# Kernel optimization log

Hardware: AMD Instinct MI355X
Metric: run time of the kernel (lower is better)

## Reference

```python
import jax, jax.numpy as jnp
import numpy as np

D = 1024
H = 16
HD = D // H
FF = 4 * D
EPS = 1e-6


def layernorm(x, g, b):
    mu = jnp.mean(x, axis=-1, keepdims=True)
    var = jnp.mean((x - mu) ** 2, axis=-1, keepdims=True)
    return (x - mu) * jax.lax.rsqrt(var + EPS) * g + b


def setup_inputs() -> dict:
    key = jax.random.key(0)
    ks = jax.random.split(key, 12)
    s = 0.02
    return {
        "x": jax.random.normal(ks[0], (8, 1024, D), dtype=jnp.float32),
        "qkv_w": jax.random.normal(ks[1], (3 * D, D), dtype=jnp.float32) * s,
        "qkv_b": jnp.zeros((3 * D,), dtype=jnp.float32),
        "proj_w": jax.random.normal(ks[2], (D, D), dtype=jnp.float32) * s,
        "proj_b": jnp.zeros((D,), dtype=jnp.float32),
        "fc1_w": jax.random.normal(ks[3], (FF, D), dtype=jnp.float32) * s,
        "fc1_b": jnp.zeros((FF,), dtype=jnp.float32),
        "fc2_w": jax.random.normal(ks[4], (D, FF), dtype=jnp.float32) * s,
        "fc2_b": jnp.zeros((D,), dtype=jnp.float32),
        "ln1_g": jnp.ones((D,), dtype=jnp.float32),
        "ln1_b": jnp.zeros((D,), dtype=jnp.float32),
        "ln2_g": jnp.ones((D,), dtype=jnp.float32),
        "ln2_b": jnp.zeros((D,), dtype=jnp.float32),
    }


def reference(x, qkv_w, qkv_b, proj_w, proj_b, fc1_w, fc1_b, fc2_w, fc2_b,
              ln1_g, ln1_b, ln2_g, ln2_b):
    B, S, _ = x.shape
    # attention branch
    h = layernorm(x, ln1_g, ln1_b)
    qkv = h @ qkv_w.T + qkv_b                      # [B,S,3D]
    qkv = qkv.reshape(B, S, 3, H, HD)
    q, k, v = qkv[:, :, 0], qkv[:, :, 1], qkv[:, :, 2]  # [B,S,H,HD]
    scores = jnp.einsum('bshd,bthd->bhst', q, k) * (HD ** -0.5)
    attn = jax.nn.softmax(scores, axis=-1)
    ctx = jnp.einsum('bhst,bthd->bshd', attn, v).reshape(B, S, D)
    x = x + ctx @ proj_w.T + proj_b
    # mlp branch
    h = layernorm(x, ln2_g, ln2_b)
    h = jax.nn.gelu(h @ fc1_w.T + fc1_b, approximate=False)
    x = x + h @ fc2_w.T + fc2_b
    return x
```

## Files before the change

kernel.cpp:

```cpp
#include <hip/hip_runtime.h>
#include <stdint.h>

typedef unsigned short u16;
typedef __attribute__((ext_vector_type(8))) short bf16x8;
typedef __attribute__((ext_vector_type(4))) short bf16x4;
typedef __attribute__((ext_vector_type(4))) float f32x4;

__device__ __forceinline__ u16 f2bf(float f) {
    union { float f; uint32_t u; } v; v.f = f;
    uint32_t r = (v.u + 0x7FFFu + ((v.u >> 16) & 1u)) >> 16;
    return (u16)r;
}

__device__ __forceinline__ void g2l16(const u16* g, u16* l) {
    __builtin_amdgcn_global_load_lds(
        (const __attribute__((address_space(1))) uint32_t*)g,
        (__attribute__((address_space(3))) uint32_t*)l, 16, 0, 0);
}

__device__ __forceinline__ float gelu_f(float x) {
    float x2 = x * x;
    float u = x * (0.7978845608028654f + 0.035677408136300125f * x2);
    float t = exp2f(-2.8853900817779268f * fabsf(u));
    float th = (1.0f - t) / (1.0f + t);
    th = (u < 0.0f) ? -th : th;
    return 0.5f * x * (1.0f + th);
}

__global__ __launch_bounds__(256) void cvt_kernel(const float* __restrict__ in,
                                                  u16* __restrict__ out, int n4) {
    int i = blockIdx.x * 256 + threadIdx.x;
    if (i < n4) {
        float4 v = ((const float4*)in)[i];
        uint2 o;
        o.x = (uint32_t)f2bf(v.x) | ((uint32_t)f2bf(v.y) << 16);
        o.y = (uint32_t)f2bf(v.z) | ((uint32_t)f2bf(v.w) << 16);
        ((uint2*)out)[i] = o;
    }
}

__global__ __launch_bounds__(256) void ln_kernel(const float* __restrict__ x,
                                                 const float* __restrict__ g,
                                                 const float* __restrict__ beta,
                                                 u16* __restrict__ out) {
    int row = blockIdx.x;
    int tid = threadIdx.x;
    const float4 v = ((const float4*)(x + (size_t)row * 1024))[tid];
    float s  = v.x + v.y + v.z + v.w;
    float sq = v.x*v.x + v.y*v.y + v.z*v.z + v.w*v.w;
    #pragma unroll
    for (int off = 32; off; off >>= 1) {
        s  += __shfl_xor(s,  off, 64);
        sq += __shfl_xor(sq, off, 64);
    }
    __shared__ float rs[4], rq[4];
    int w = tid >> 6;
    if ((tid & 63) == 0) { rs[w] = s; rq[w] = sq; }
    __syncthreads();
    s  = rs[0] + rs[1] + rs[2] + rs[3];
    sq = rq[0] + rq[1] + rq[2] + rq[3];
    float mu   = s * (1.0f / 1024.0f);
    float var  = sq * (1.0f / 1024.0f) - mu * mu;
    float rstd = rsqrtf(var + 1e-6f);
    float4 gv = ((const float4*)g)[tid];
    float4 bv = ((const float4*)beta)[tid];
    uint2 o;
    o.x = (uint32_t)f2bf((v.x - mu) * rstd * gv.x + bv.x) |
          ((uint32_t)f2bf((v.y - mu) * rstd * gv.y + bv.y) << 16);
    o.y = (uint32_t)f2bf((v.z - mu) * rstd * gv.z + bv.z) |
          ((uint32_t)f2bf((v.w - mu) * rstd * gv.w + bv.w) << 16);
    ((uint2*)(out + (size_t)row * 1024))[tid] = o;
}

template<int M_REP, int ACT, int RES, int OUTBF>
__global__ __launch_bounds__(512, 2) void gemm2_kernel(
    const u16* __restrict__ A, const u16* __restrict__ W,
    const float* __restrict__ bias, const float* __restrict__ res,
    void* __restrict__ Cout, int M, int N, int K)
{
    const int BM = M_REP * 32;
    __shared__ u16 sA[2 * BM * 64];
    __shared__ u16 sB[2 * 256 * 64];

    int tid = threadIdx.x;
    int lane = tid & 63, wid = tid >> 6;
    int wm = wid >> 2, wn = wid & 3;
    int q = lane & 15, g = lane >> 4;

    int MT = M / BM;
    int nwg = gridDim.x;
    int chunk = nwg >> 3;
    int bid = blockIdx.x;
    int wg = (bid & 7) * chunk + (bid >> 3);
    int mt = wg % MT, nt = wg / MT;
    int m0 = mt * BM, n0 = nt * 256;

    const int NT = K >> 6;

    f32x4 acc[M_REP][4] = {};

    auto STAGE = [&](int buf, int k0) {
        #pragma unroll
        for (int l = 0; l < BM / 64; l++) {
            int idx = l * 512 + tid;
            int row = idx >> 3;
            int col = ((idx & 7) * 8) ^ ((row & 7) << 3);
            g2l16(A + (size_t)(m0 + row) * K + k0 + col,
                  sA + buf * (BM * 64) + (l * 512 + wid * 64) * 8);
        }
        #pragma unroll
        for (int l = 0; l < 4; l++) {
            int idx = l * 512 + tid;
            int row = idx >> 3;
            int col = ((idx & 7) * 8) ^ ((row & 7) << 3);
            g2l16(W + (size_t)(n0 + row) * K + k0 + col,
                  sB + buf * (256 * 64) + (l * 512 + wid * 64) * 8);
        }
    };

    STAGE(0, 0);
    __syncthreads();

    int buf = 0;
    for (int t = 0; t < NT; t++) {
        if (t + 1 < NT) STAGE(buf ^ 1, (t + 1) << 6);
        const u16* bA = sA + buf * (BM * 64);
        const u16* bB = sB + buf * (256 * 64);
        #pragma unroll
        for (int ks = 0; ks < 2; ks++) {
            bf16x8 af[M_REP], bfr[4];
            #pragma unroll
            for (int i = 0; i < M_REP; i++) {
                int rowL = wm * (BM / 2) + i * 16 + q;
                int colE = (ks * 32 + g * 8) ^ ((rowL & 7) << 3);
                af[i] = *(const bf16x8*)(bA + rowL * 64 + colE);
            }
            #pragma unroll
            for (int j = 0; j < 4; j++) {
                int rowL = wn * 64 + j * 16 + q;
                int colE = (ks * 32 + g * 8) ^ ((rowL & 7) << 3);
                bfr[j] = *(const bf16x8*)(bB + rowL * 64 + colE);
            }
            #pragma unroll
            for (int i = 0; i < M_REP; i++)
                #pragma unroll
                for (int j = 0; j < 4; j++)
                    acc[i][j] = __builtin_amdgcn_mfma_f32_16x16x32_bf16(af[i], bfr[j], acc[i][j], 0, 0, 0);
        }
        __syncthreads();
        buf ^= 1;
    }

    #pragma unroll
    for (int i = 0; i < M_REP; i++) {
        #pragma unroll
        for (int j = 0; j < 4; j++) {
            int col = n0 + wn * 64 + j * 16 + q;
            float bz = bias[col];
            #pragma unroll
            for (int r = 0; r < 4; r++) {
                int row = m0 + wm * (BM / 2) + i * 16 + g * 4 + r;
                float v = acc[i][j][r] + bz;
                if (ACT == 1) v = gelu_f(v);
                if (RES) v += res[(size_t)row * N + col];
                if (OUTBF) ((u16*)Cout)[(size_t)row * N + col] = f2bf(v);
                else       ((float*)Cout)[(size_t)row * N + col] = v;
            }
        }
    }
}

__global__ __launch_bounds__(256) void attn_kernel(const u16* __restrict__ qkv,
                                                   u16* __restrict__ ctx) {
    int bid = blockIdx.x;
    int qt = bid & 15;
    int h  = (bid >> 4) & 15;
    int b  = bid >> 8;
    int tid = threadIdx.x, lane = tid & 63, w = tid >> 6;
    int q = lane & 15, g = lane >> 4;

    __shared__ u16 sQ[64 * 72];
    __shared__ u16 sK[32 * 72];
    __shared__ u16 sVT[64 * 36];

    const size_t tokBase = ((size_t)b * 1024) * 3072 + (size_t)h * 64;
    const float SC = 0.125f * 1.44269504088896f;

    #pragma unroll
    for (int p = 0; p < 2; p++) {
        int flat = (p * 256 + tid) * 8;
        int r = flat >> 6, c = flat & 63;
        uint4 v = *(const uint4*)(qkv + tokBase + (size_t)(qt * 64 + r) * 3072 + c);
        *(uint4*)(sQ + r * 72 + c) = v;
    }
    __syncthreads();
    bf16x8 qf0 = *(const bf16x8*)(sQ + (w * 16 + q) * 72 + g * 8);
    bf16x8 qf1 = *(const bf16x8*)(sQ + (w * 16 + q) * 72 + 32 + g * 8);

    float m_run = -1e30f, l_run = 0.0f;
    f32x4 o[4];
    #pragma unroll
    for (int n = 0; n < 4; n++) o[n] = (f32x4){0.f, 0.f, 0.f, 0.f};

    int kr = tid >> 3, kc = (tid & 7) * 8;
    int kperm = ((kr >> 2) & 3) * 8 + (kr >> 4) * 4 + (kr & 3);

    for (int kt = 0; kt < 32; kt++) {
        __syncthreads();
        {
            uint4 v = *(const uint4*)(qkv + tokBase + (size_t)(kt * 32 + kperm) * 3072 + 1024 + kc);
            *(uint4*)(sK + kr * 72 + kc) = v;
        }
        #pragma unroll
        for (int p = 0; p < 2; p++) {
            int flat = (p * 256 + tid) * 4;
            int key = flat >> 6, cc = flat & 63;
            ushort4 vv = *(const ushort4*)(qkv + tokBase + (size_t)(kt * 32 + key) * 3072 + 2048 + cc);
            sVT[(cc + 0) * 36 + key] = vv.x;
            sVT[(cc + 1) * 36 + key] = vv.y;
            sVT[(cc + 2) * 36 + key] = vv.z;
            sVT[(cc + 3) * 36 + key] = vv.w;
        }
        __syncthreads();

        f32x4 s0 = (f32x4){0.f, 0.f, 0.f, 0.f}, s1 = s0;
        {
            bf16x8 k00 = *(const bf16x8*)(sK + (q) * 72 + g * 8);
            bf16x8 k01 = *(const bf16x8*)(sK + (q) * 72 + 32 + g * 8);
            s0 = __builtin_amdgcn_mfma_f32_16x16x32_bf16(k00, qf0, s0, 0, 0, 0);
            s0 = __builtin_amdgcn_mfma_f32_16x16x32_bf16(k01, qf1, s0, 0, 0, 0);
            bf16x8 k10 = *(const bf16x8*)(sK + (16 + q) * 72 + g * 8);
            bf16x8 k11 = *(const bf16x8*)(sK + (16 + q) * 72 + 32 + g * 8);
            s1 = __builtin_amdgcn_mfma_f32_16x16x32_bf16(k10, qf0, s1, 0, 0, 0);
            s1 = __builtin_amdgcn_mfma_f32_16x16x32_bf16(k11, qf1, s1, 0, 0, 0);
        }
        float ps[8];
        #pragma unroll
        for (int r = 0; r < 4; r++) { ps[r] = s0[r] * SC; ps[4 + r] = s1[r] * SC; }
        float tm = ps[0];
        #pragma unroll
        for (int i = 1; i < 8; i++) tm = fmaxf(tm, ps[i]);
        tm = fmaxf(tm, __shfl_xor(tm, 16, 64));
        tm = fmaxf(tm, __shfl_xor(tm, 32, 64));

        if (!__all(tm - m_run <= 8.0f)) {
            float nm = fmaxf(m_run, tm);
            float f = exp2f(m_run - nm);
            float fr[4];
            #pragma unroll
            for (int r = 0; r < 4; r++) fr[r] = __shfl(f, g * 4 + r, 64);
            #pragma unroll
            for (int n = 0; n < 4; n++)
                #pragma unroll
                for (int r = 0; r < 4; r++) o[n][r] *= fr[r];
            l_run *= f;
            m_run = nm;
        }

        float ts = 0.0f;
        #pragma unroll
        for (int i = 0; i < 8; i++) { ps[i] = exp2f(ps[i] - m_run); ts += ps[i]; }
        ts += __shfl_xor(ts, 16, 64);
        ts += __shfl_xor(ts, 32, 64);
        l_run += ts;

        bf16x8 pf;
        #pragma unroll
        for (int j = 0; j < 8; j++) pf[j] = (short)f2bf(ps[j]);

        #pragma unroll
        for (int n = 0; n < 4; n++) {
            bf16x4 vlo = *(const bf16x4*)(sVT + (n * 16 + q) * 36 + g * 8);
            bf16x4 vhi = *(const bf16x4*)(sVT + (n * 16 + q) * 36 + g * 8 + 4);
            bf16x8 vf;
            #pragma unroll
            for (int j = 0; j < 4; j++) { vf[j] = vlo[j]; vf[4 + j] = vhi[j]; }
            o[n] = __builtin_amdgcn_mfma_f32_16x16x32_bf16(pf, vf, o[n], 0, 0, 0);
        }
    }

    float inv = 1.0f / l_run;
    float ir[4];
    #pragma unroll
    for (int r = 0; r < 4; r++) ir[r] = __shfl(inv, g * 4 + r, 64);
    size_t outBase = ((size_t)b * 1024 + qt * 64 + w * 16) * 1024 + (size_t)h * 64;
    #pragma unroll
    for (int n = 0; n < 4; n++)
        #pragma unroll
        for (int r = 0; r < 4; r++)
            ctx[outBase + (size_t)(g * 4 + r) * 1024 + n * 16 + q] = f2bf(o[n][r] * ir[r]);
}

extern "C" void kernel_launch(void* const* d_in, const int* in_sizes, int n_in,
                              void* d_out, int out_size, void* d_ws, size_t ws_size,
                              hipStream_t stream) {
    const float* x      = (const float*)d_in[0];
    const float* qkv_w  = (const float*)d_in[1];
    const float* qkv_b  = (const float*)d_in[2];
    const float* proj_w = (const float*)d_in[3];
    const float* proj_b = (const float*)d_in[4];
    const float* fc1_w  = (const float*)d_in[5];
    const float* fc1_b  = (const float*)d_in[6];
    const float* fc2_w  = (const float*)d_in[7];
    const float* fc2_b  = (const float*)d_in[8];
    const float* ln1_g  = (const float*)d_in[9];
    const float* ln1_b  = (const float*)d_in[10];
    const float* ln2_g  = (const float*)d_in[11];
    const float* ln2_b  = (const float*)d_in[12];
    float* out = (float*)d_out;

    char* ws = (char*)d_ws;
    u16* wq = (u16*)(ws);
    u16* wp = (u16*)(ws + 6291456);
    u16* w1 = (u16*)(ws + 8388608);
    u16* w2 = (u16*)(ws + 16777216);
    char* pool = ws + 25165824;
    u16* hbuf = (u16*)(pool);
    u16* qkvb = (u16*)(pool + 16777216);
    u16* ctxb = (u16*)(pool);
    u16* h2b  = (u16*)(pool + 16777216);
    u16* a1b  = (u16*)(pool + 33554432);

    cvt_kernel<<<3072, 256, 0, stream>>>(qkv_w, wq, 786432);
    cvt_kernel<<<1024, 256, 0, stream>>>(proj_w, wp, 262144);
    cvt_kernel<<<4096, 256, 0, stream>>>(fc1_w, w1, 1048576);
    cvt_kernel<<<4096, 256, 0, stream>>>(fc2_w, w2, 1048576);

    ln_kernel<<<8192, 256, 0, stream>>>(x, ln1_g, ln1_b, hbuf);
    gemm2_kernel<4,0,0,1><<<768, 512, 0, stream>>>(hbuf, wq, qkv_b, nullptr, qkvb, 8192, 3072, 1024);
    attn_kernel<<<2048, 256, 0, stream>>>(qkvb, ctxb);
    gemm2_kernel<4,0,1,0><<<256, 512, 0, stream>>>(ctxb, wp, proj_b, x, out, 8192, 1024, 1024);
    ln_kernel<<<8192, 256, 0, stream>>>(out, ln2_g, ln2_b, h2b);
    gemm2_kernel<8,1,0,1><<<512, 512, 0, stream>>>(h2b, w1, fc1_b, nullptr, a1b, 8192, 4096, 1024);
    gemm2_kernel<4,0,1,0><<<256, 512, 0, stream>>>(a1b, w2, fc2_b, out, out, 8192, 1024, 4096);
}
```

Before: 563.2 us.

## Triple-stage GEMM prefetch, write V transposed from QKV GEMM, double-buffer attention tiles

The GEMM now issues the loads for stage t+2 right after the fragments are read, using explicit waitcnt and barriers in place of a single-stage prefetch. The tile is fixed at 128x256, so the fc1 GEMM drops from 256-row tiles to 128-row tiles with twice the workgroups, and the occupancy hint of two workgroups per CU is removed. The QKV GEMM epilogue writes V transposed into a separate buffer, so attention no longer does a scalar LDS transpose. Attention processes 64-key tiles with register-staged double buffering of K and V. The risks are hand-managed vmcnt counts, more register pressure, and scattered 8-byte stores when writing the transposed V.

```diff
diff --git a/kernel.cpp b/kernel.cpp
--- a/kernel.cpp
+++ b/kernel.cpp
@@ -3,7 +3,6 @@
 
 typedef unsigned short u16;
 typedef __attribute__((ext_vector_type(8))) short bf16x8;
-typedef __attribute__((ext_vector_type(4))) short bf16x4;
 typedef __attribute__((ext_vector_type(4))) float f32x4;
 
 __device__ __forceinline__ u16 f2bf(float f) {
@@ -72,105 +71,135 @@
     ((uint2*)(out + (size_t)row * 1024))[tid] = o;
 }
 
-template<int M_REP, int ACT, int RES, int OUTBF>
-__global__ __launch_bounds__(512, 2) void gemm2_kernel(
+template<int ACT, int RES, int OUTMODE>
+__global__ __launch_bounds__(512) void gemm2_kernel(
     const u16* __restrict__ A, const u16* __restrict__ W,
     const float* __restrict__ bias, const float* __restrict__ res,
-    void* __restrict__ Cout, int M, int N, int K)
+    void* __restrict__ Cout, u16* __restrict__ vtb, int M, int N, int K)
 {
-    const int BM = M_REP * 32;
-    __shared__ u16 sA[2 * BM * 64];
-    __shared__ u16 sB[2 * 256 * 64];
+    const int BM = 128, BN = 256, BK = 64;
+    __shared__ u16 sA[2 * BM * BK];
+    __shared__ u16 sB[2 * BN * BK];
 
     int tid = threadIdx.x;
     int lane = tid & 63, wid = tid >> 6;
     int wm = wid >> 2, wn = wid & 3;
     int q = lane & 15, g = lane >> 4;
 
-    int MT = M / BM;
+    int MT = M >> 7;
     int nwg = gridDim.x;
     int chunk = nwg >> 3;
     int bid = blockIdx.x;
     int wg = (bid & 7) * chunk + (bid >> 3);
     int mt = wg % MT, nt = wg / MT;
-    int m0 = mt * BM, n0 = nt * 256;
-
+    int m0 = mt << 7, n0 = nt << 8;
     const int NT = K >> 6;
 
-    f32x4 acc[M_REP][4] = {};
-
-    auto STAGE = [&](int buf, int k0) {
-        #pragma unroll
-        for (int l = 0; l < BM / 64; l++) {
-            int idx = l * 512 + tid;
-            int row = idx >> 3;
-            int col = ((idx & 7) * 8) ^ ((row & 7) << 3);
-            g2l16(A + (size_t)(m0 + row) * K + k0 + col,
-                  sA + buf * (BM * 64) + (l * 512 + wid * 64) * 8);
-        }
-        #pragma unroll
-        for (int l = 0; l < 4; l++) {
-            int idx = l * 512 + tid;
-            int row = idx >> 3;
-            int col = ((idx & 7) * 8) ^ ((row & 7) << 3);
-            g2l16(W + (size_t)(n0 + row) * K + k0 + col,
-                  sB + buf * (256 * 64) + (l * 512 + wid * 64) * 8);
-        }
-    };
+    const u16* srcA[2]; const u16* srcB[4];
+    u16* dstA[2]; u16* dstB[4];
+    #pragma unroll
+    for (int l = 0; l < 2; l++) {
+        int idx = l * 512 + tid, row = idx >> 3;
+        int col = ((idx & 7) * 8) ^ ((row & 7) << 3);
+        srcA[l] = A + (size_t)(m0 + row) * K + col;
+        dstA[l] = sA + (l * 512 + wid * 64) * 8;
+    }
+    #pragma unroll
+    for (int l = 0; l < 4; l++) {
+        int idx = l * 512 + tid, row = idx >> 3;
+        int col = ((idx & 7) * 8) ^ ((row & 7) << 3);
+        srcB[l] = W + (size_t)(n0 + row) * K + col;
+        dstB[l] = sB + (l * 512 + wid * 64) * 8;
+    }
+
+    #define STAGE(bf, t) { int ko = (t) * 64; int boA = (bf) * (BM * BK); int boB = (bf) * (BN * BK); \
+        g2l16(srcA[0] + ko, dstA[0] + boA); g2l16(srcA[1] + ko, dstA[1] + boA); \
+        g2l16(srcB[0] + ko, dstB[0] + boB); g2l16(srcB[1] + ko, dstB[1] + boB); \
+        g2l16(srcB[2] + ko, dstB[2] + boB); g2l16(srcB[3] + ko, dstB[3] + boB); }
+
+    f32x4 acc[4][4] = {};
 
     STAGE(0, 0);
-    __syncthreads();
+    STAGE(1, 1);
+    asm volatile("s_waitcnt vmcnt(6)\n" ::: "memory");
+    __builtin_amdgcn_s_barrier();
 
     int buf = 0;
     for (int t = 0; t < NT; t++) {
-        if (t + 1 < NT) STAGE(buf ^ 1, (t + 1) << 6);
-        const u16* bA = sA + buf * (BM * 64);
-        const u16* bB = sB + buf * (256 * 64);
+        const u16* bA = sA + buf * (BM * BK);
+        const u16* bB = sB + buf * (BN * BK);
+        bf16x8 af[2][4], bfr[2][4];
         #pragma unroll
         for (int ks = 0; ks < 2; ks++) {
-            bf16x8 af[M_REP], bfr[4];
-            #pragma unroll
-            for (int i = 0; i < M_REP; i++) {
-                int rowL = wm * (BM / 2) + i * 16 + q;
+            #pragma unroll
+            for (int i = 0; i < 4; i++) {
+                int rowL = wm * 64 + i * 16 + q;
                 int colE = (ks * 32 + g * 8) ^ ((rowL & 7) << 3);
-                af[i] = *(const bf16x8*)(bA + rowL * 64 + colE);
+                af[ks][i] = *(const bf16x8*)(bA + rowL * 64 + colE);
             }
             #pragma unroll
             for (int j = 0; j < 4; j++) {
                 int rowL = wn * 64 + j * 16 + q;
                 int colE = (ks * 32 + g * 8) ^ ((rowL & 7) << 3);
-                bfr[j] = *(const bf16x8*)(bB + rowL * 64 + colE);
+                bfr[ks][j] = *(const bf16x8*)(bB + rowL * 64 + colE);
             }
-            #pragma unroll
-            for (int i = 0; i < M_REP; i++)
+        }
+        asm volatile("s_waitcnt lgkmcnt(0)\n" ::: "memory");
+        __builtin_amdgcn_s_barrier();
+        bool pre = (t + 2 < NT);
+        if (pre) STAGE(buf, t + 2);
+        #pragma unroll
+        for (int ks = 0; ks < 2; ks++)
+            #pragma unroll
+            for (int i = 0; i < 4; i++)
                 #pragma unroll
                 for (int j = 0; j < 4; j++)
-                    acc[i][j] = __builtin_amdgcn_mfma_f32_16x16x32_bf16(af[i], bfr[j], acc[i][j], 0, 0, 0);
-        }
-        __syncthreads();
+                    acc[i][j] = __builtin_amdgcn_mfma_f32_16x16x32_bf16(af[ks][i], bfr[ks][j], acc[i][j], 0, 0, 0);
+        if (pre) { asm volatile("s_waitcnt vmcnt(6)\n" ::: "memory"); }
+        else     { asm volatile("s_waitcnt vmcnt(0)\n" ::: "memory"); }
+        __builtin_amdgcn_s_barrier();
         buf ^= 1;
     }
-
-    #pragma unroll
-    for (int i = 0; i < M_REP; i++) {
+    #undef STAGE
+
+    #pragma unroll
+    for (int i = 0; i < 4; i++) {
         #pragma unroll
         for (int j = 0; j < 4; j++) {
             int col = n0 + wn * 64 + j * 16 + q;
             float bz = bias[col];
+            int row0 = m0 + wm * 64 + i * 16 + g * 4;
+            float vv[4];
             #pragma unroll
             for (int r = 0; r < 4; r++) {
-                int row = m0 + wm * (BM / 2) + i * 16 + g * 4 + r;
                 float v = acc[i][j][r] + bz;
                 if (ACT == 1) v = gelu_f(v);
-                if (RES) v += res[(size_t)row * N + col];
-                if (OUTBF) ((u16*)Cout)[(size_t)row * N + col] = f2bf(v);
-                else       ((float*)Cout)[(size_t)row * N + col] = v;
+                if (RES) v += res[(size_t)(row0 + r) * N + col];
+                vv[r] = v;
             }
-        }
-    }
-}
-
-__global__ __launch_bounds__(256) void attn_kernel(const u16* __restrict__ qkv,
+            if (OUTMODE == 0) {
+                #pragma unroll
+                for (int r = 0; r < 4; r++) ((float*)Cout)[(size_t)(row0 + r) * N + col] = vv[r];
+            } else if (OUTMODE == 1) {
+                #pragma unroll
+                for (int r = 0; r < 4; r++) ((u16*)Cout)[(size_t)(row0 + r) * N + col] = f2bf(vv[r]);
+            } else {
+                if (col < 2048) {
+                    #pragma unroll
+                    for (int r = 0; r < 4; r++) ((u16*)Cout)[(size_t)(row0 + r) * 2048 + col] = f2bf(vv[r]);
+                } else {
+                    int hd = col & 63, hh = (col >> 6) - 32;
+                    int b_ = row0 >> 10, s_ = row0 & 1023;
+                    ushort4 pk = { f2bf(vv[0]), f2bf(vv[1]), f2bf(vv[2]), f2bf(vv[3]) };
+                    *(ushort4*)(vtb + (((size_t)(b_ * 16 + hh) * 64 + hd) << 10) + s_) = pk;
+                }
+            }
+        }
+    }
+}
+
+__global__ __launch_bounds__(256) void attn_kernel(const u16* __restrict__ qk,
+                                                   const u16* __restrict__ vt,
                                                    u16* __restrict__ ctx) {
     int bid = blockIdx.x;
     int qt = bid & 15;
@@ -179,67 +208,67 @@
     int tid = threadIdx.x, lane = tid & 63, w = tid >> 6;
     int q = lane & 15, g = lane >> 4;
 
-    __shared__ u16 sQ[64 * 72];
-    __shared__ u16 sK[32 * 72];
-    __shared__ u16 sVT[64 * 36];
-
-    const size_t tokBase = ((size_t)b * 1024) * 3072 + (size_t)h * 64;
+    __shared__ u16 sK[2][64 * 72];
+    __shared__ u16 sV[2][64 * 72];
+
+    const size_t tokBase = (size_t)b * 1024 * 2048 + (size_t)h * 64;
+    const u16* vbase = vt + (size_t)(b * 16 + h) * 64 * 1024;
     const float SC = 0.125f * 1.44269504088896f;
 
-    #pragma unroll
-    for (int p = 0; p < 2; p++) {
-        int flat = (p * 256 + tid) * 8;
-        int r = flat >> 6, c = flat & 63;
-        uint4 v = *(const uint4*)(qkv + tokBase + (size_t)(qt * 64 + r) * 3072 + c);
-        *(uint4*)(sQ + r * 72 + c) = v;
+    const u16* qrow = qk + tokBase + (size_t)(qt * 64 + w * 16 + q) * 2048;
+    bf16x8 qf0 = *(const bf16x8*)(qrow + g * 8);
+    bf16x8 qf1 = *(const bf16x8*)(qrow + 32 + g * 8);
+
+    int r0 = tid >> 3, c0 = (tid & 7) * 8;
+    int kp0 = 8 * ((r0 >> 2) & 3) + 4 * ((r0 >> 4) & 1) + (r0 & 3);
+    int kp1 = 32 + kp0;
+
+    {
+        uint4 k0 = *(const uint4*)(qk + tokBase + (size_t)kp0 * 2048 + 1024 + c0);
+        uint4 k1 = *(const uint4*)(qk + tokBase + (size_t)kp1 * 2048 + 1024 + c0);
+        uint4 v0 = *(const uint4*)(vbase + (size_t)r0 * 1024 + c0);
+        uint4 v1 = *(const uint4*)(vbase + (size_t)(32 + r0) * 1024 + c0);
+        *(uint4*)(&sK[0][r0 * 72 + c0]) = k0;
+        *(uint4*)(&sK[0][(32 + r0) * 72 + c0]) = k1;
+        *(uint4*)(&sV[0][r0 * 72 + c0]) = v0;
+        *(uint4*)(&sV[0][(32 + r0) * 72 + c0]) = v1;
     }
     __syncthreads();
-    bf16x8 qf0 = *(const bf16x8*)(sQ + (w * 16 + q) * 72 + g * 8);
-    bf16x8 qf1 = *(const bf16x8*)(sQ + (w * 16 + q) * 72 + 32 + g * 8);
 
     float m_run = -1e30f, l_run = 0.0f;
     f32x4 o[4];
     #pragma unroll
     for (int n = 0; n < 4; n++) o[n] = (f32x4){0.f, 0.f, 0.f, 0.f};
 
-    int kr = tid >> 3, kc = (tid & 7) * 8;
-    int kperm = ((kr >> 2) & 3) * 8 + (kr >> 4) * 4 + (kr & 3);
-
-    for (int kt = 0; kt < 32; kt++) {
-        __syncthreads();
-        {
-            uint4 v = *(const uint4*)(qkv + tokBase + (size_t)(kt * 32 + kperm) * 3072 + 1024 + kc);
-            *(uint4*)(sK + kr * 72 + kc) = v;
-        }
-        #pragma unroll
-        for (int p = 0; p < 2; p++) {
-            int flat = (p * 256 + tid) * 4;
-            int key = flat >> 6, cc = flat & 63;
-            ushort4 vv = *(const ushort4*)(qkv + tokBase + (size_t)(kt * 32 + key) * 3072 + 2048 + cc);
-            sVT[(cc + 0) * 36 + key] = vv.x;
-            sVT[(cc + 1) * 36 + key] = vv.y;
-            sVT[(cc + 2) * 36 + key] = vv.z;
-            sVT[(cc + 3) * 36 + key] = vv.w;
-        }
-        __syncthreads();
-
-        f32x4 s0 = (f32x4){0.f, 0.f, 0.f, 0.f}, s1 = s0;
-        {
-            bf16x8 k00 = *(const bf16x8*)(sK + (q) * 72 + g * 8);
-            bf16x8 k01 = *(const bf16x8*)(sK + (q) * 72 + 32 + g * 8);
-            s0 = __builtin_amdgcn_mfma_f32_16x16x32_bf16(k00, qf0, s0, 0, 0, 0);
-            s0 = __builtin_amdgcn_mfma_f32_16x16x32_bf16(k01, qf1, s0, 0, 0, 0);
-            bf16x8 k10 = *(const bf16x8*)(sK + (16 + q) * 72 + g * 8);
-            bf16x8 k11 = *(const bf16x8*)(sK + (16 + q) * 72 + 32 + g * 8);
-            s1 = __builtin_amdgcn_mfma_f32_16x16x32_bf16(k10, qf0, s1, 0, 0, 0);
-            s1 = __builtin_amdgcn_mfma_f32_16x16x32_bf16(k11, qf1, s1, 0, 0, 0);
-        }
-        float ps[8];
-        #pragma unroll
-        for (int r = 0; r < 4; r++) { ps[r] = s0[r] * SC; ps[4 + r] = s1[r] * SC; }
+    for (int kt = 0; kt < 16; kt++) {
+        int cur = kt & 1;
+        uint4 kn0 = {}, kn1 = {}, vn0 = {}, vn1 = {};
+        if (kt < 15) {
+            size_t kb = tokBase + (size_t)((kt + 1) * 64) * 2048 + 1024 + c0;
+            kn0 = *(const uint4*)(qk + kb + (size_t)kp0 * 2048);
+            kn1 = *(const uint4*)(qk + kb + (size_t)kp1 * 2048);
+            vn0 = *(const uint4*)(vbase + (size_t)r0 * 1024 + (kt + 1) * 64 + c0);
+            vn1 = *(const uint4*)(vbase + (size_t)(32 + r0) * 1024 + (kt + 1) * 64 + c0);
+        }
+
+        f32x4 s[4];
+        #pragma unroll
+        for (int c = 0; c < 4; c++) {
+            s[c] = (f32x4){0.f, 0.f, 0.f, 0.f};
+            bf16x8 a0 = *(const bf16x8*)(&sK[cur][(c * 16 + q) * 72 + g * 8]);
+            bf16x8 a1 = *(const bf16x8*)(&sK[cur][(c * 16 + q) * 72 + 32 + g * 8]);
+            s[c] = __builtin_amdgcn_mfma_f32_16x16x32_bf16(a0, qf0, s[c], 0, 0, 0);
+            s[c] = __builtin_amdgcn_mfma_f32_16x16x32_bf16(a1, qf1, s[c], 0, 0, 0);
+        }
+        float ps[16];
+        #pragma unroll
+        for (int c = 0; c < 4; c++)
+            #pragma unroll
+            for (int r = 0; r < 4; r++) ps[c * 4 + r] = s[c][r] * SC;
+
         float tm = ps[0];
         #pragma unroll
-        for (int i = 1; i < 8; i++) tm = fmaxf(tm, ps[i]);
+        for (int i = 1; i < 16; i++) tm = fmaxf(tm, ps[i]);
         tm = fmaxf(tm, __shfl_xor(tm, 16, 64));
         tm = fmaxf(tm, __shfl_xor(tm, 32, 64));
 
@@ -259,24 +288,38 @@
 
         float ts = 0.0f;
         #pragma unroll
-        for (int i = 0; i < 8; i++) { ps[i] = exp2f(ps[i] - m_run); ts += ps[i]; }
+        for (int i = 0; i < 16; i++) { ps[i] = exp2f(ps[i] - m_run); ts += ps[i]; }
         ts += __shfl_xor(ts, 16, 64);
         ts += __shfl_xor(ts, 32, 64);
         l_run += ts;
 
-        bf16x8 pf;
-        #pragma unroll
-        for (int j = 0; j < 8; j++) pf[j] = (short)f2bf(ps[j]);
+        bf16x8 pf0, pf1;
+        #pragma unroll
+        for (int j = 0; j < 4; j++) {
+            pf0[j]     = (short)f2bf(ps[j]);
+            pf0[4 + j] = (short)f2bf(ps[4 + j]);
+            pf1[j]     = (short)f2bf(ps[8 + j]);
+            pf1[4 + j] = (short)f2bf(ps[12 + j]);
+        }
+
+        if (kt < 15) {
+            *(uint4*)(&sK[cur ^ 1][r0 * 72 + c0]) = kn0;
+            *(uint4*)(&sK[cur ^ 1][(32 + r0) * 72 + c0]) = kn1;
+            *(uint4*)(&sV[cur ^ 1][r0 * 72 + c0]) = vn0;
+            *(uint4*)(&sV[cur ^ 1][(32 + r0) * 72 + c0]) = vn1;
+        }
 
         #pragma unroll
         for (int n = 0; n < 4; n++) {
-            bf16x4 vlo = *(const bf16x4*)(sVT + (n * 16 + q) * 36 + g * 8);
-            bf16x4 vhi = *(const bf16x4*)(sVT + (n * 16 + q) * 36 + g * 8 + 4);
-            bf16x8 vf;
-            #pragma unroll
-            for (int j = 0; j < 4; j++) { vf[j] = vlo[j]; vf[4 + j] = vhi[j]; }
-            o[n] = __builtin_amdgcn_mfma_f32_16x16x32_bf16(pf, vf, o[n], 0, 0, 0);
-        }
+            bf16x8 v0 = *(const bf16x8*)(&sV[cur][(n * 16 + q) * 72 + g * 8]);
+            o[n] = __builtin_amdgcn_mfma_f32_16x16x32_bf16(pf0, v0, o[n], 0, 0, 0);
+        }
+        #pragma unroll
+        for (int n = 0; n < 4; n++) {
+            bf16x8 v1 = *(const bf16x8*)(&sV[cur][(n * 16 + q) * 72 + 32 + g * 8]);
+            o[n] = __builtin_amdgcn_mfma_f32_16x16x32_bf16(pf1, v1, o[n], 0, 0, 0);
+        }
+        __syncthreads();
     }
 
     float inv = 1.0f / l_run;
@@ -316,7 +359,8 @@
     u16* w2 = (u16*)(ws + 16777216);
     char* pool = ws + 25165824;
     u16* hbuf = (u16*)(pool);
-    u16* qkvb = (u16*)(pool + 16777216);
+    u16* qkb  = (u16*)(pool + 16777216);
+    u16* vtb  = (u16*)(pool + 50331648);
     u16* ctxb = (u16*)(pool);
     u16* h2b  = (u16*)(pool + 16777216);
     u16* a1b  = (u16*)(pool + 33554432);
@@ -327,10 +371,10 @@
     cvt_kernel<<<4096, 256, 0, stream>>>(fc2_w, w2, 1048576);
 
     ln_kernel<<<8192, 256, 0, stream>>>(x, ln1_g, ln1_b, hbuf);
-    gemm2_kernel<4,0,0,1><<<768, 512, 0, stream>>>(hbuf, wq, qkv_b, nullptr, qkvb, 8192, 3072, 1024);
-    attn_kernel<<<2048, 256, 0, stream>>>(qkvb, ctxb);
-    gemm2_kernel<4,0,1,0><<<256, 512, 0, stream>>>(ctxb, wp, proj_b, x, out, 8192, 1024, 1024);
+    gemm2_kernel<0,0,2><<<768, 512, 0, stream>>>(hbuf, wq, qkv_b, nullptr, qkb, vtb, 8192, 3072, 1024);
+    attn_kernel<<<2048, 256, 0, stream>>>(qkb, vtb, ctxb);
+    gemm2_kernel<0,1,0><<<256, 512, 0, stream>>>(ctxb, wp, proj_b, x, out, nullptr, 8192, 1024, 1024);
     ln_kernel<<<8192, 256, 0, stream>>>(out, ln2_g, ln2_b, h2b);
-    gemm2_kernel<8,1,0,1><<<512, 512, 0, stream>>>(h2b, w1, fc1_b, nullptr, a1b, 8192, 4096, 1024);
-    gemm2_kernel<4,0,1,0><<<256, 512, 0, stream>>>(a1b, w2, fc2_b, out, out, 8192, 1024, 4096);
-}
+    gemm2_kernel<1,0,1><<<1024, 512, 0, stream>>>(h2b, w1, fc1_b, nullptr, a1b, nullptr, 8192, 4096, 1024);
+    gemm2_kernel<0,1,0><<<256, 512, 0, stream>>>(a1b, w2, fc2_b, out, out, nullptr, 8192, 1024, 4096);
+}
```

After: 530.0 us. 1.06x faster.
